# Performance work log

Hardware: AMD Instinct MI355X
Metric: run time of the kernel (lower is better)

Reference implementation:

```python
import jax, jax.numpy as jnp
import numpy as np

H, C = 8, 16            # heads, per-head channels (at_channels)
HID = H * C             # 128
N_NODES = 50000
N_EDGES = 400000
N_GRAPHS = 500
SPEC = 1000


def setup_inputs() -> dict:
    key = jax.random.key(0)
    ks = jax.random.split(key, 32)
    s = 0.05

    def rn(k, shape):
        return jax.random.normal(k, shape, jnp.float32) * s

    inp = {}
    inp["x"] = jax.random.normal(ks[0], (N_NODES, 16), jnp.float32)
    inp["edge_index"] = jax.random.randint(ks[1], (2, N_EDGES), 0, N_NODES, jnp.int32)
    inp["edge_attr"] = jax.random.normal(ks[2], (N_EDGES, 2), jnp.float32)
    inp["batch"] = jnp.sort(jax.random.randint(ks[3], (N_NODES,), 0, N_GRAPHS, jnp.int32))
    # layer 1 (input dim 16)
    inp["at1_Wl"] = rn(ks[4], (16, HID)); inp["at1_bl"] = rn(ks[5], (HID,))
    inp["at1_Wr"] = rn(ks[6], (16, HID)); inp["at1_br"] = rn(ks[7], (HID,))
    inp["at1_We"] = rn(ks[8], (2, HID))
    inp["at1_att"] = rn(ks[9], (H, C))
    inp["at1_bias"] = rn(ks[10], (HID,))
    inp["l1_W"] = rn(ks[11], (16, HID)); inp["l1_b"] = rn(ks[12], (HID,))
    # layers 2..10 stacked (input dim 128)
    inp["atk_Wl"] = rn(ks[13], (9, HID, HID)); inp["atk_bl"] = rn(ks[14], (9, HID))
    inp["atk_Wr"] = rn(ks[15], (9, HID, HID)); inp["atk_br"] = rn(ks[16], (9, HID))
    inp["atk_We"] = rn(ks[17], (9, 2, HID))
    inp["atk_att"] = rn(ks[18], (9, H, C))
    inp["atk_bias"] = rn(ks[19], (9, HID))
    inp["lk_W"] = rn(ks[20], (9, HID, HID)); inp["lk_b"] = rn(ks[21], (9, HID))
    # readout
    inp["lin_W"] = rn(ks[22], (HID, SPEC)); inp["lin_b"] = rn(ks[23], (SPEC,))
    return inp


def _gatv2(x, src, dst, eattr, Wl, bl, Wr, br, We, att, bias):
    """PyG GATv2Conv forward (concat=True, slope=0.2, self-loops already in src/dst)."""
    N = x.shape[0]
    xl = (x @ Wl + bl).reshape(N, H, C)   # source transform
    xr = (x @ Wr + br).reshape(N, H, C)   # target transform
    ee = (eattr @ We).reshape(-1, H, C)   # edge embedding
    m = xl[src] + xr[dst] + ee            # [E, H, C]
    m = jnp.where(m > 0, m, 0.2 * m)      # leaky_relu
    logits = jnp.einsum('ehc,hc->eh', m, att)
    mx = jax.ops.segment_max(logits, dst, num_segments=N)
    ea = jnp.exp(logits - mx[dst])
    denom = jax.ops.segment_sum(ea, dst, num_segments=N)
    alpha = ea / jnp.maximum(denom[dst], 1e-16)
    out = jax.ops.segment_sum(xl[src] * alpha[:, :, None], dst, num_segments=N)
    return out.reshape(N, HID) + bias


def reference(x, edge_index, edge_attr, batch,
              at1_Wl, at1_bl, at1_Wr, at1_br, at1_We, at1_att, at1_bias, l1_W, l1_b,
              atk_Wl, atk_bl, atk_Wr, atk_br, atk_We, atk_att, atk_bias, lk_W, lk_b,
              lin_W, lin_b):
    N = x.shape[0]
    # add self loops once (edge_attr fill_value='mean', PyG default)
    sl = jnp.arange(N, dtype=edge_index.dtype)
    src = jnp.concatenate([edge_index[0], sl])
    dst = jnp.concatenate([edge_index[1], sl])
    ea = jnp.concatenate([edge_attr, jnp.broadcast_to(edge_attr.mean(0), (N, edge_attr.shape[1]))])

    h = jax.nn.elu(_gatv2(x, src, dst, ea, at1_Wl, at1_bl, at1_Wr, at1_br,
                          at1_We, at1_att, at1_bias) + x @ l1_W + l1_b)
    for i in range(9):  # layers 2..10
        h = jax.nn.elu(_gatv2(h, src, dst, ea, atk_Wl[i], atk_bl[i], atk_Wr[i], atk_br[i],
                              atk_We[i], atk_att[i], atk_bias[i]) + h @ lk_W[i] + lk_b[i])

    # global mean pool over graphs
    sums = jax.ops.segment_sum(h, batch, num_segments=N_GRAPHS)
    cnts = jax.ops.segment_sum(jnp.ones((N, 1), h.dtype), batch, num_segments=N_GRAPHS)
    g = sums / jnp.maximum(cnts, 1.0)
    return g @ lin_W + lin_b
```

## Files before the change

### kernel.cpp

```cpp
#include <hip/hip_runtime.h>
#include <hip/hip_bf16.h>
#include <cstdint>

#define HID 128

typedef __attribute__((ext_vector_type(8))) short bf16x8;
typedef __attribute__((ext_vector_type(4))) float f32x4;

__device__ __forceinline__ unsigned short f2bf(float x) {
    __hip_bfloat16 h = __float2bfloat16(x);
    return __builtin_bit_cast(unsigned short, h);
}
__device__ __forceinline__ float bf2f(unsigned short u) {
    return __bfloat162float(__builtin_bit_cast(__hip_bfloat16, u));
}
__device__ __forceinline__ float bflo(unsigned u) {
    return __builtin_bit_cast(float, u << 16);
}
__device__ __forceinline__ float bfhi(unsigned u) {
    return __builtin_bit_cast(float, u & 0xffff0000u);
}
__device__ __forceinline__ float4 ld4bf(const unsigned short* p) {
    ushort4 u = *(const ushort4*)p;
    return make_float4(bf2f(u.x), bf2f(u.y), bf2f(u.z), bf2f(u.w));
}
__device__ __forceinline__ int lower_bound_i(const int* a, int n, int v) {
    int lo = 0, hi = n;
    while (lo < hi) { int m = (lo + hi) >> 1; if (a[m] < v) lo = m + 1; else hi = m; }
    return lo;
}

__global__ __launch_bounds__(256) void mean_kernel(const float* __restrict__ eattr,
                                                   float* __restrict__ meansum, int E) {
    float sx = 0.f, sy = 0.f;
    for (int i = blockIdx.x * 256 + threadIdx.x; i < E; i += gridDim.x * 256) {
        float2 v = *(const float2*)(eattr + 2 * (size_t)i);
        sx += v.x; sy += v.y;
    }
    for (int d = 1; d < 64; d <<= 1) { sx += __shfl_xor(sx, d); sy += __shfl_xor(sy, d); }
    if ((threadIdx.x & 63) == 0) { atomicAdd(&meansum[0], sx); atomicAdd(&meansum[1], sy); }
}

__global__ __launch_bounds__(256) void deg_kernel(const int* __restrict__ ei,
                                                  int* __restrict__ deg, int E, int ET) {
    int e = blockIdx.x * 256 + threadIdx.x;
    if (e >= ET) return;
    int dst = (e < E) ? ei[E + e] : (e - E);
    atomicAdd(&deg[dst], 1);
}

__global__ __launch_bounds__(256) void scanA_kernel(const int* __restrict__ deg,
                                                    int* __restrict__ bsum, int N) {
    __shared__ int ws[4];
    int t = threadIdx.x;
    int base = blockIdx.x * 1024 + t * 4;
    int s = 0;
    #pragma unroll
    for (int j = 0; j < 4; j++) { int idx = base + j; if (idx < N) s += deg[idx]; }
    for (int d = 1; d < 64; d <<= 1) s += __shfl_xor(s, d);
    if ((t & 63) == 0) ws[t >> 6] = s;
    __syncthreads();
    if (t == 0) bsum[blockIdx.x] = ws[0] + ws[1] + ws[2] + ws[3];
}

__global__ __launch_bounds__(64) void scanB_kernel(const int* __restrict__ bsum,
                                                   int* __restrict__ boff,
                                                   int* __restrict__ row_ptr, int NB, int N) {
    int t = threadIdx.x;
    int v = (t < NB) ? bsum[t] : 0;
    int inc = v;
    #pragma unroll
    for (int d = 1; d < 64; d <<= 1) { int u = __shfl_up(inc, d); if (t >= d) inc += u; }
    if (t < NB) boff[t] = inc - v;
    if (t == 63) row_ptr[N] = inc;
}

__global__ __launch_bounds__(256) void scanC_kernel(const int* __restrict__ deg,
                                                    const int* __restrict__ boff,
                                                    int* __restrict__ row_ptr,
                                                    int* __restrict__ cursor, int N) {
    __shared__ int wsum[4];
    int t = threadIdx.x;
    int lane = t & 63, wid = t >> 6;
    int base = blockIdx.x * 1024 + t * 4;
    int v[4]; int s = 0;
    #pragma unroll
    for (int j = 0; j < 4; j++) { int idx = base + j; v[j] = (idx < N) ? deg[idx] : 0; s += v[j]; }
    int inc = s;
    #pragma unroll
    for (int d = 1; d < 64; d <<= 1) { int u = __shfl_up(inc, d); if (lane >= d) inc += u; }
    if (lane == 63) wsum[wid] = inc;
    __syncthreads();
    int woff = 0;
    for (int ww = 0; ww < wid; ww++) woff += wsum[ww];
    int excl = boff[blockIdx.x] + woff + inc - s;
    #pragma unroll
    for (int j = 0; j < 4; j++) {
        int idx = base + j;
        if (idx < N) { row_ptr[idx] = excl; cursor[idx] = excl; }
        excl += v[j];
    }
}

__global__ __launch_bounds__(256) void fill_kernel(const int* __restrict__ ei,
                                                   const float* __restrict__ eattr,
                                                   const float* __restrict__ meansum,
                                                   int* __restrict__ cursor,
                                                   int* __restrict__ csr_src,
                                                   unsigned int* __restrict__ csr_eap,
                                                   int E, int ET) {
    int e = blockIdx.x * 256 + threadIdx.x;
    if (e >= ET) return;
    int src, dst; float2 ea;
    if (e < E) {
        src = ei[e]; dst = ei[E + e];
        ea = *(const float2*)(eattr + 2 * (size_t)e);
    } else {
        src = dst = e - E;
        float inv = 1.0f / (float)E;
        ea.x = meansum[0] * inv; ea.y = meansum[1] * inv;
    }
    unsigned pea = (unsigned)f2bf(ea.x) | ((unsigned)f2bf(ea.y) << 16);
    int pos = atomicAdd(&cursor[dst], 1);
    csr_src[pos] = src;
    csr_eap[pos] = pea;
}

__global__ __launch_bounds__(256) void wprep_kernel(const float* __restrict__ src,
                                                    unsigned short* __restrict__ hi, int total) {
    int idx = blockIdx.x * 256 + threadIdx.x;
    if (idx >= total) return;
    int layer = idx >> 14;
    int rem = idx & 16383;
    int n = rem >> 7, k = rem & 127;
    hi[idx] = f2bf(src[(layer << 14) | (k << 7) | n]);
}

#define LROW 136
__global__ __launch_bounds__(256) void gemm3_kernel(
    const unsigned short* __restrict__ Hb,
    const unsigned short* __restrict__ W0h, const float* __restrict__ b0, unsigned short* __restrict__ o0,
    const unsigned short* __restrict__ W1h, const float* __restrict__ b1, unsigned short* __restrict__ o1,
    const unsigned short* __restrict__ W2h, const float* __restrict__ b2, unsigned short* __restrict__ o2,
    int N) {
    __shared__ unsigned short lds_h[128 * LROW];
    int tid = threadIdx.x;
    int wid = tid >> 6, lane = tid & 63;
    int row0 = blockIdx.x * 64 + wid * 16;
    int lr = lane & 15;
    int cgrp = lane >> 4;
    int kb = cgrp * 8;
    bool rowsok = (row0 < N);

    bf16x8 ha[4];
    {
        int node = row0 + lr;
        int nodec = rowsok ? ((node < N) ? node : (N - 1)) : 0;
        const unsigned short* pa = Hb + (size_t)nodec * HID + kb;
        #pragma unroll
        for (int kf = 0; kf < 4; kf++) ha[kf] = *(const bf16x8*)(pa + kf * 32);
    }

    const unsigned short* Whs[3] = {W0h, W1h, W2h};
    const float* Bs[3] = {b0, b1, b2};
    unsigned short* Os[3] = {o0, o1, o2};

    for (int w = 0; w < 3; w++) {
        if (w) __syncthreads();
        const unsigned short* sh = Whs[w];
        #pragma unroll
        for (int j = 0; j < 8; j++) {
            int c = tid + 256 * j;
            int r = c >> 4, col = (c & 15) * 8;
            *(bf16x8*)&lds_h[r * LROW + col] = *(const bf16x8*)(sh + r * HID + col);
        }
        __syncthreads();
        if (!rowsok) continue;

        const float* bias = Bs[w];
        unsigned short* outp = Os[w];
        #pragma unroll 2
        for (int nf = 0; nf < 8; nf++) {
            int wrow = nf * 16 + lr;
            const unsigned short* ph = &lds_h[wrow * LROW + kb];
            bf16x8 wf[4];
            #pragma unroll
            for (int kf = 0; kf < 4; kf++) wf[kf] = *(const bf16x8*)(ph + kf * 32);
            f32x4 acc = {0.f, 0.f, 0.f, 0.f};
            #pragma unroll
            for (int kf = 0; kf < 4; kf++)
                acc = __builtin_amdgcn_mfma_f32_16x16x32_bf16(wf[kf], ha[kf], acc, 0, 0, 0);
            int chb = nf * 16 + cgrp * 4;
            float4 bias4 = *(const float4*)(bias + chb);
            int node = row0 + lr;
            ushort4 u;
            u.x = f2bf(acc[0] + bias4.x); u.y = f2bf(acc[1] + bias4.y);
            u.z = f2bf(acc[2] + bias4.z); u.w = f2bf(acc[3] + bias4.w);
            if (node < N) *(ushort4*)(outp + (size_t)node * HID + chb) = u;
        }
    }
}

__global__ __launch_bounds__(256) void transform16_kernel(
    const float* __restrict__ Hin,
    const float* __restrict__ W0, const float* __restrict__ b0, float* __restrict__ o0,
    const float* __restrict__ W1, const float* __restrict__ b1, float* __restrict__ o1,
    int N) {
    constexpr int K = 16;
    __shared__ float Ws[K][HID];
    __shared__ float Hs[32][K + 4];

    const float* W; const float* bias; float* outp;
    if (blockIdx.z == 0) { W = W0; bias = b0; outp = o0; }
    else                 { W = W1; bias = b1; outp = o1; }

    int row0 = blockIdx.x * 32;
    int tid = threadIdx.x;
    int tx = tid & 15, ty = tid >> 4;

    for (int i = tid; i < 32 * (K / 4); i += 256) {
        int r = i / (K / 4), kq = i % (K / 4);
        int row = row0 + r;
        float4 v = make_float4(0.f, 0.f, 0.f, 0.f);
        if (row < N) v = *(const float4*)(Hin + (size_t)row * K + kq * 4);
        *(float4*)&Hs[r][kq * 4] = v;
    }
    for (int i = tid; i < K * 32; i += 256) {
        int k = i >> 5, cq = i & 31;
        *(float4*)&Ws[k][cq * 4] = *(const float4*)(W + (size_t)k * HID + cq * 4);
    }
    __syncthreads();

    float acc[2][8];
    #pragma unroll
    for (int i = 0; i < 2; i++)
        #pragma unroll
        for (int j = 0; j < 8; j++) acc[i][j] = 0.f;

    int r0 = ty * 2, r1 = ty * 2 + 1;
    #pragma unroll
    for (int k = 0; k < K; k++) {
        float a0 = Hs[r0][k];
        float a1 = Hs[r1][k];
        float4 w0 = *(float4*)&Ws[k][tx * 4];
        float4 w1 = *(float4*)&Ws[k][64 + tx * 4];
        acc[0][0] += a0 * w0.x; acc[0][1] += a0 * w0.y; acc[0][2] += a0 * w0.z; acc[0][3] += a0 * w0.w;
        acc[0][4] += a0 * w1.x; acc[0][5] += a0 * w1.y; acc[0][6] += a0 * w1.z; acc[0][7] += a0 * w1.w;
        acc[1][0] += a1 * w0.x; acc[1][1] += a1 * w0.y; acc[1][2] += a1 * w0.z; acc[1][3] += a1 * w0.w;
        acc[1][4] += a1 * w1.x; acc[1][5] += a1 * w1.y; acc[1][6] += a1 * w1.z; acc[1][7] += a1 * w1.w;
    }

    float4 bb0 = *(const float4*)(bias + tx * 4);
    float4 bb1 = *(const float4*)(bias + 64 + tx * 4);
    #pragma unroll
    for (int i = 0; i < 2; i++) {
        int row = row0 + ty * 2 + i;
        if (row < N) {
            float4 v0 = make_float4(acc[i][0] + bb0.x, acc[i][1] + bb0.y, acc[i][2] + bb0.z, acc[i][3] + bb0.w);
            float4 v1 = make_float4(acc[i][4] + bb1.x, acc[i][5] + bb1.y, acc[i][6] + bb1.z, acc[i][7] + bb1.w);
            *(float4*)(outp + (size_t)row * HID + tx * 4) = v0;
            *(float4*)(outp + (size_t)row * HID + 64 + tx * 4) = v1;
        }
    }
}

__global__ __launch_bounds__(256) void combine16_kernel(
    const float* __restrict__ Hin,
    const float* __restrict__ W, const float* __restrict__ bias,
    const float* __restrict__ Att, unsigned short* __restrict__ Hb,
    int N) {
    constexpr int K = 16;
    __shared__ float Ws[K][HID];
    __shared__ float Hs[32][K + 4];

    int row0 = blockIdx.x * 32;
    int tid = threadIdx.x;
    int tx = tid & 15, ty = tid >> 4;

    for (int i = tid; i < 32 * (K / 4); i += 256) {
        int r = i / (K / 4), kq = i % (K / 4);
        int row = row0 + r;
        float4 v = make_float4(0.f, 0.f, 0.f, 0.f);
        if (row < N) v = *(const float4*)(Hin + (size_t)row * K + kq * 4);
        *(float4*)&Hs[r][kq * 4] = v;
    }
    for (int i = tid; i < K * 32; i += 256) {
        int k = i >> 5, cq = i & 31;
        *(float4*)&Ws[k][cq * 4] = *(const float4*)(W + (size_t)k * HID + cq * 4);
    }
    __syncthreads();

    float acc[2][8];
    #pragma unroll
    for (int i = 0; i < 2; i++)
        #pragma unroll
        for (int j = 0; j < 8; j++) acc[i][j] = 0.f;

    int r0 = ty * 2, r1 = ty * 2 + 1;
    #pragma unroll
    for (int k = 0; k < K; k++) {
        float a0 = Hs[r0][k];
        float a1 = Hs[r1][k];
        float4 w0 = *(float4*)&Ws[k][tx * 4];
        float4 w1 = *(float4*)&Ws[k][64 + tx * 4];
        acc[0][0] += a0 * w0.x; acc[0][1] += a0 * w0.y; acc[0][2] += a0 * w0.z; acc[0][3] += a0 * w0.w;
        acc[0][4] += a0 * w1.x; acc[0][5] += a0 * w1.y; acc[0][6] += a0 * w1.z; acc[0][7] += a0 * w1.w;
        acc[1][0] += a1 * w0.x; acc[1][1] += a1 * w0.y; acc[1][2] += a1 * w0.z; acc[1][3] += a1 * w0.w;
        acc[1][4] += a1 * w1.x; acc[1][5] += a1 * w1.y; acc[1][6] += a1 * w1.z; acc[1][7] += a1 * w1.w;
    }

    float4 bb0 = *(const float4*)(bias + tx * 4);
    float4 bb1 = *(const float4*)(bias + 64 + tx * 4);
    #pragma unroll
    for (int i = 0; i < 2; i++) {
        int row = row0 + ty * 2 + i;
        if (row < N) {
            const float* p0 = Att + (size_t)row * HID + tx * 4;
            float4 g0 = *(const float4*)p0;
            float4 g1 = *(const float4*)(p0 + 64);
            float v[8];
            v[0] = g0.x + acc[i][0] + bb0.x; v[1] = g0.y + acc[i][1] + bb0.y;
            v[2] = g0.z + acc[i][2] + bb0.z; v[3] = g0.w + acc[i][3] + bb0.w;
            v[4] = g1.x + acc[i][4] + bb1.x; v[5] = g1.y + acc[i][5] + bb1.y;
            v[6] = g1.z + acc[i][6] + bb1.z; v[7] = g1.w + acc[i][7] + bb1.w;
            #pragma unroll
            for (int j = 0; j < 8; j++) v[j] = (v[j] > 0.f) ? v[j] : (__expf(v[j]) - 1.f);
            ushort4 h0, h1;
            h0.x = f2bf(v[0]); h0.y = f2bf(v[1]); h0.z = f2bf(v[2]); h0.w = f2bf(v[3]);
            h1.x = f2bf(v[4]); h1.y = f2bf(v[5]); h1.z = f2bf(v[6]); h1.w = f2bf(v[7]);
            *(ushort4*)(Hb + (size_t)row * HID + tx * 4) = h0;
            *(ushort4*)(Hb + (size_t)row * HID + 64 + tx * 4) = h1;
        }
    }
}

template <int FUSE>
__global__ __launch_bounds__(256) void edge_kernel(
    const void* __restrict__ XLv, const void* __restrict__ XRv,
    const int* __restrict__ row_ptr, const int* __restrict__ csr_src,
    const unsigned int* __restrict__ csr_eap,
    const float* __restrict__ att,
    const float* __restrict__ We,
    const float* __restrict__ gbias,
    const unsigned short* __restrict__ lin,
    float* __restrict__ hf, unsigned short* __restrict__ hb,
    int N) {
    int n = (blockIdx.x * 256 + threadIdx.x) >> 6;
    int lane = threadIdx.x & 63;
    int half = lane >> 5;
    int l = lane & 31;
    bool active = (n < N);
    int nn = active ? n : 0;

    int c0 = l * 4;
    float4 av  = *(const float4*)(att + c0);
    float4 we0 = *(const float4*)(We + c0);
    float4 we1 = *(const float4*)(We + HID + c0);

    auto ldx = [&](const void* p, int idx) -> float4 {
        if constexpr (FUSE) return ld4bf((const unsigned short*)p + (size_t)idx * HID + c0);
        else                return *(const float4*)((const float*)p + (size_t)idx * HID + c0);
    };
    float4 xr = ldx(XRv, nn);

    int eb = 0, eend = 0;
    if (active) { eb = row_ptr[n]; eend = row_ptr[n + 1]; }
    int mid = (eb + eend + 1) >> 1;
    int sb = half ? mid : eb;
    int se = half ? eend : mid;

    float l_run = 0.f;
    float4 fa = make_float4(0.f, 0.f, 0.f, 0.f);

    for (int base = sb; base < se; base += 32) {
        int cnt = min(32, se - base);
        int myi = base + l;
        int msrc = 0; unsigned mea = 0;
        if (myi < se) { msrc = csr_src[myi]; mea = csr_eap[myi]; }

        int s0 = __shfl(msrc, 0, 32);
        int s1 = __shfl(msrc, 1, 32);
        unsigned e0 = __shfl(mea, 0, 32);
        unsigned e1 = __shfl(mea, 1, 32);
        float4 xl0 = ldx(XLv, s0);
        float4 xl1 = ldx(XLv, s1);

        for (int j = 0; ; j += 2) {
            bool more = (j + 2 < cnt);
            int ns0 = 0, ns1 = 0; unsigned ne0 = 0, ne1 = 0;
            float4 nxl0, nxl1;
            if (more) {
                ns0 = __shfl(msrc, j + 2, 32);
                ns1 = __shfl(msrc, j + 3, 32);
                ne0 = __shfl(mea, j + 2, 32);
                ne1 = __shfl(mea, j + 3, 32);
                nxl0 = ldx(XLv, ns0);
                nxl1 = ldx(XLv, ns1);
            }
            float ex0 = bflo(e0), ey0 = bfhi(e0);
            float ex1 = bflo(e1), ey1 = bfhi(e1);
            float t, part0, part1;
            float m0x = xl0.x + xr.x + ex0 * we0.x + ey0 * we1.x;
            float m0y = xl0.y + xr.y + ex0 * we0.y + ey0 * we1.y;
            float m0z = xl0.z + xr.z + ex0 * we0.z + ey0 * we1.z;
            float m0w = xl0.w + xr.w + ex0 * we0.w + ey0 * we1.w;
            m0x = fmaxf(m0x, 0.2f * m0x);
            m0y = fmaxf(m0y, 0.2f * m0y);
            m0z = fmaxf(m0z, 0.2f * m0z);
            m0w = fmaxf(m0w, 0.2f * m0w);
            part0 = m0x * av.x + m0y * av.y + m0z * av.z + m0w * av.w;
            float m1x = xl1.x + xr.x + ex1 * we0.x + ey1 * we1.x;
            float m1y = xl1.y + xr.y + ex1 * we0.y + ey1 * we1.y;
            float m1z = xl1.z + xr.z + ex1 * we0.z + ey1 * we1.z;
            float m1w = xl1.w + xr.w + ex1 * we0.w + ey1 * we1.w;
            m1x = fmaxf(m1x, 0.2f * m1x);
            m1y = fmaxf(m1y, 0.2f * m1y);
            m1z = fmaxf(m1z, 0.2f * m1z);
            m1w = fmaxf(m1w, 0.2f * m1w);
            part1 = m1x * av.x + m1y * av.y + m1z * av.z + m1w * av.w;
            t = __shfl_xor(part0, 1); part0 += t;
            t = __shfl_xor(part0, 2); part0 += t;
            t = __shfl_xor(part1, 1); part1 += t;
            t = __shfl_xor(part1, 2); part1 += t;

            bool two = (j + 1 < cnt);
            float p0 = __expf(fminf(part0, 60.f));
            float p1 = two ? __expf(fminf(part1, 60.f)) : 0.f;
            l_run += p0 + p1;
            fa.x += p0 * xl0.x + p1 * xl1.x;
            fa.y += p0 * xl0.y + p1 * xl1.y;
            fa.z += p0 * xl0.z + p1 * xl1.z;
            fa.w += p0 * xl0.w + p1 * xl1.w;
            if (!more) break;
            s0 = ns0; s1 = ns1; e0 = ne0; e1 = ne1; xl0 = nxl0; xl1 = nxl1;
        }
    }

    l_run += __shfl_xor(l_run, 32);
    fa.x += __shfl_xor(fa.x, 32);
    fa.y += __shfl_xor(fa.y, 32);
    fa.z += __shfl_xor(fa.z, 32);
    fa.w += __shfl_xor(fa.w, 32);

    if (!active || half) return;
    float inv = 1.f / fmaxf(l_run, 1e-16f);
    float4 bias4 = *(const float4*)(gbias + c0);
    float4 v;
    v.x = fa.x * inv + bias4.x;
    v.y = fa.y * inv + bias4.y;
    v.z = fa.z * inv + bias4.z;
    v.w = fa.w * inv + bias4.w;
    if constexpr (FUSE) {
        float4 lv = ld4bf(lin + (size_t)n * HID + c0);
        v.x += lv.x; v.y += lv.y; v.z += lv.z; v.w += lv.w;
        v.x = (v.x > 0.f) ? v.x : (__expf(v.x) - 1.f);
        v.y = (v.y > 0.f) ? v.y : (__expf(v.y) - 1.f);
        v.z = (v.z > 0.f) ? v.z : (__expf(v.z) - 1.f);
        v.w = (v.w > 0.f) ? v.w : (__expf(v.w) - 1.f);
        if (hf) *(float4*)(hf + (size_t)n * HID + c0) = v;
        ushort4 hh;
        hh.x = f2bf(v.x); hh.y = f2bf(v.y); hh.z = f2bf(v.z); hh.w = f2bf(v.w);
        *(ushort4*)(hb + (size_t)n * HID + c0) = hh;
    } else {
        *(float4*)(hf + (size_t)n * HID + c0) = v;
    }
}

__global__ __launch_bounds__(128) void pool_kernel(const float* __restrict__ h,
                                                   const int* __restrict__ batch,
                                                   float* __restrict__ g, int N) {
    int gid = blockIdx.x;
    int lo = lower_bound_i(batch, N, gid);
    int hi = lower_bound_i(batch, N, gid + 1);
    int c = threadIdx.x;
    float s = 0.f;
    for (int i = lo; i < hi; i++) s += h[(size_t)i * HID + c];
    g[gid * HID + c] = s / fmaxf((float)(hi - lo), 1.0f);
}

__global__ __launch_bounds__(256) void readout_kernel(const float* __restrict__ g,
                                                      const float* __restrict__ W,
                                                      const float* __restrict__ b,
                                                      float* __restrict__ out, int S) {
    __shared__ float gs[HID];
    int gid = blockIdx.y;
    if (threadIdx.x < HID) gs[threadIdx.x] = g[gid * HID + threadIdx.x];
    __syncthreads();
    int c = blockIdx.x * 256 + threadIdx.x;
    if (c < S) {
        float acc = b[c];
        #pragma unroll 8
        for (int k = 0; k < HID; k++) acc += gs[k] * W[(size_t)k * S + c];
        out[(size_t)gid * S + c] = acc;
    }
}

extern "C" void kernel_launch(void* const* d_in, const int* in_sizes, int n_in,
                              void* d_out, int out_size, void* d_ws, size_t ws_size,
                              hipStream_t stream) {
    const float* x      = (const float*)d_in[0];
    const int*   ei     = (const int*)d_in[1];
    const float* eattr  = (const float*)d_in[2];
    const int*   batch  = (const int*)d_in[3];
    const float* at1_Wl = (const float*)d_in[4];
    const float* at1_bl = (const float*)d_in[5];
    const float* at1_Wr = (const float*)d_in[6];
    const float* at1_br = (const float*)d_in[7];
    const float* at1_We = (const float*)d_in[8];
    const float* at1_att= (const float*)d_in[9];
    const float* at1_b  = (const float*)d_in[10];
    const float* l1_W   = (const float*)d_in[11];
    const float* l1_b   = (const float*)d_in[12];
    const float* atk_Wl = (const float*)d_in[13];
    const float* atk_bl = (const float*)d_in[14];
    const float* atk_Wr = (const float*)d_in[15];
    const float* atk_br = (const float*)d_in[16];
    const float* atk_We = (const float*)d_in[17];
    const float* atk_att= (const float*)d_in[18];
    const float* atk_b  = (const float*)d_in[19];
    const float* lk_W   = (const float*)d_in[20];
    const float* lk_b   = (const float*)d_in[21];
    const float* lin_W  = (const float*)d_in[22];
    const float* lin_b  = (const float*)d_in[23];
    float* out = (float*)d_out;

    const int N  = in_sizes[0] / 16;
    const int E  = in_sizes[1] / 2;
    const int ET = E + N;
    const int S  = 1000;
    const int G  = out_size / S;

    char* w = (char*)d_ws;
    auto alloc = [&](size_t bytes) -> char* {
        char* p = w; w += (bytes + 255) & ~(size_t)255; return p;
    };
    float*  XLf     = (float*)alloc((size_t)N * HID * 4);
    float*  XRf     = (float*)alloc((size_t)N * HID * 4);
    unsigned short* XLb = (unsigned short*)alloc((size_t)N * HID * 2);
    unsigned short* XRb = (unsigned short*)alloc((size_t)N * HID * 2);
    unsigned short* Linb = (unsigned short*)alloc((size_t)N * HID * 2);
    float*  Hf      = (float*)alloc((size_t)N * HID * 4);
    unsigned short* Hb = (unsigned short*)alloc((size_t)N * HID * 2);
    int*    deg     = (int*)alloc((size_t)N * 4);
    int*    row_ptr = (int*)alloc((size_t)(N + 1) * 4);
    int*    cursor  = (int*)alloc((size_t)N * 4);
    int*    csr_src = (int*)alloc((size_t)ET * 4);
    unsigned int* csr_eap = (unsigned int*)alloc((size_t)ET * 4);
    float*  meansum = (float*)alloc(8);
    int*    bsum    = (int*)alloc(256);
    int*    boff    = (int*)alloc(256);
    unsigned short* WlTh = (unsigned short*)alloc((size_t)9 * 16384 * 2);
    unsigned short* WrTh = (unsigned short*)alloc((size_t)9 * 16384 * 2);
    unsigned short* WkTh = (unsigned short*)alloc((size_t)9 * 16384 * 2);
    float*  gpool   = (float*)alloc((size_t)G * HID * 4);
    (void)ws_size; (void)n_in;

    hipMemsetAsync(deg, 0, (size_t)N * 4, stream);
    hipMemsetAsync(meansum, 0, 8, stream);

    const int wtot = 9 * 16384;
    wprep_kernel<<<(wtot + 255) / 256, 256, 0, stream>>>(atk_Wl, WlTh, wtot);
    wprep_kernel<<<(wtot + 255) / 256, 256, 0, stream>>>(atk_Wr, WrTh, wtot);
    wprep_kernel<<<(wtot + 255) / 256, 256, 0, stream>>>(lk_W,   WkTh, wtot);

    mean_kernel<<<256, 256, 0, stream>>>(eattr, meansum, E);
    deg_kernel<<<(ET + 255) / 256, 256, 0, stream>>>(ei, deg, E, ET);
    const int NB = (N + 1023) / 1024;
    scanA_kernel<<<NB, 256, 0, stream>>>(deg, bsum, N);
    scanB_kernel<<<1, 64, 0, stream>>>(bsum, boff, row_ptr, NB, N);
    scanC_kernel<<<NB, 256, 0, stream>>>(deg, boff, row_ptr, cursor, N);
    fill_kernel<<<(ET + 255) / 256, 256, 0, stream>>>(ei, eattr, meansum, cursor, csr_src, csr_eap, E, ET);

    const int gx16 = (N + 31) / 32;
    const int ge   = (N + 3) / 4;
    const int gx3  = (N + 63) / 64;

    transform16_kernel<<<dim3(gx16, 1, 2), 256, 0, stream>>>(x, at1_Wl, at1_bl, XLf, at1_Wr, at1_br, XRf, N);
    edge_kernel<0><<<ge, 256, 0, stream>>>(XLf, XRf, row_ptr, csr_src, csr_eap, at1_att, at1_We, at1_b,
                                           nullptr, Hf, nullptr, N);
    combine16_kernel<<<gx16, 256, 0, stream>>>(x, l1_W, l1_b, Hf, Hb, N);

    for (int i = 0; i < 9; i++) {
        const unsigned short* wlh = WlTh + (size_t)i * 16384;
        const unsigned short* wrh = WrTh + (size_t)i * 16384;
        const unsigned short* wkh = WkTh + (size_t)i * 16384;
        const float* bl = atk_bl + (size_t)i * HID;
        const float* br = atk_br + (size_t)i * HID;
        const float* bk = lk_b   + (size_t)i * HID;
        const float* Wep = atk_We + (size_t)i * 2 * HID;
        const float* at = atk_att + (size_t)i * HID;
        const float* ab = atk_b  + (size_t)i * HID;

        gemm3_kernel<<<gx3, 256, 0, stream>>>(Hb,
                                              wlh, bl, XLb,
                                              wrh, br, XRb,
                                              wkh, bk, Linb, N);
        edge_kernel<1><<<ge, 256, 0, stream>>>(XLb, XRb, row_ptr, csr_src, csr_eap, at, Wep, ab,
                                               Linb, (i == 8) ? Hf : nullptr, Hb, N);
    }

    pool_kernel<<<G, 128, 0, stream>>>(Hf, batch, gpool, N);
    readout_kernel<<<dim3((S + 255) / 256, G), 256, 0, stream>>>(gpool, lin_W, lin_b, out, S);
}
```

Measured before the change: 754.9 us.

## Switch intermediate storage from bf16 to fp16 and use packed-half math in edge kernel

Changes all 16-bit intermediates (weights, node features, edge attributes) from bf16 to fp16 and the GEMM MFMA to the f16 variant. The edge kernel for layers 2-10 is split into its own version that computes the message, leaky-relu and attention dot product with packed half2 arithmetic and fdot2. This is meant to halve the VALU work of the per-edge logit computation. It reduces dynamic range, so large activations could overflow, and it lowers precision in the attention logits.

```diff
diff --git a/kernel.cpp b/kernel.cpp
--- a/kernel.cpp
+++ b/kernel.cpp
@@ -1,28 +1,30 @@
 #include <hip/hip_runtime.h>
-#include <hip/hip_bf16.h>
+#include <hip/hip_fp16.h>
 #include <cstdint>
 
 #define HID 128
 
-typedef __attribute__((ext_vector_type(8))) short bf16x8;
+typedef __attribute__((ext_vector_type(8))) _Float16 f16x8;
+typedef __attribute__((ext_vector_type(2))) _Float16 h2v;
 typedef __attribute__((ext_vector_type(4))) float f32x4;
 
-__device__ __forceinline__ unsigned short f2bf(float x) {
-    __hip_bfloat16 h = __float2bfloat16(x);
-    return __builtin_bit_cast(unsigned short, h);
-}
-__device__ __forceinline__ float bf2f(unsigned short u) {
-    return __bfloat162float(__builtin_bit_cast(__hip_bfloat16, u));
-}
-__device__ __forceinline__ float bflo(unsigned u) {
-    return __builtin_bit_cast(float, u << 16);
-}
-__device__ __forceinline__ float bfhi(unsigned u) {
-    return __builtin_bit_cast(float, u & 0xffff0000u);
-}
-__device__ __forceinline__ float4 ld4bf(const unsigned short* p) {
-    ushort4 u = *(const ushort4*)p;
-    return make_float4(bf2f(u.x), bf2f(u.y), bf2f(u.z), bf2f(u.w));
+__device__ __forceinline__ unsigned short f2h(float x) {
+    return __builtin_bit_cast(unsigned short, (_Float16)x);
+}
+__device__ __forceinline__ float h2f(unsigned short u) {
+    return (float)__builtin_bit_cast(_Float16, u);
+}
+__device__ __forceinline__ h2v mkh2(unsigned short a, unsigned short b) {
+    unsigned v = (unsigned)a | ((unsigned)b << 16);
+    return __builtin_bit_cast(h2v, v);
+}
+__device__ __forceinline__ h2v splath(unsigned short a) {
+    _Float16 h = __builtin_bit_cast(_Float16, a);
+    h2v r; r[0] = h; r[1] = h;
+    return r;
+}
+__device__ __forceinline__ float fdot2v(h2v a, h2v b, float c) {
+    return __builtin_amdgcn_fdot2(a, b, c, false);
 }
 __device__ __forceinline__ int lower_bound_i(const int* a, int n, int v) {
     int lo = 0, hi = n;
@@ -120,7 +122,7 @@
         float inv = 1.0f / (float)E;
         ea.x = meansum[0] * inv; ea.y = meansum[1] * inv;
     }
-    unsigned pea = (unsigned)f2bf(ea.x) | ((unsigned)f2bf(ea.y) << 16);
+    unsigned pea = (unsigned)f2h(ea.x) | ((unsigned)f2h(ea.y) << 16);
     int pos = atomicAdd(&cursor[dst], 1);
     csr_src[pos] = src;
     csr_eap[pos] = pea;
@@ -133,7 +135,7 @@
     int layer = idx >> 14;
     int rem = idx & 16383;
     int n = rem >> 7, k = rem & 127;
-    hi[idx] = f2bf(src[(layer << 14) | (k << 7) | n]);
+    hi[idx] = f2h(src[(layer << 14) | (k << 7) | n]);
 }
 
 #define LROW 136
@@ -152,13 +154,13 @@
     int kb = cgrp * 8;
     bool rowsok = (row0 < N);
 
-    bf16x8 ha[4];
+    f16x8 ha[4];
     {
         int node = row0 + lr;
         int nodec = rowsok ? ((node < N) ? node : (N - 1)) : 0;
         const unsigned short* pa = Hb + (size_t)nodec * HID + kb;
         #pragma unroll
-        for (int kf = 0; kf < 4; kf++) ha[kf] = *(const bf16x8*)(pa + kf * 32);
+        for (int kf = 0; kf < 4; kf++) ha[kf] = *(const f16x8*)(pa + kf * 32);
     }
 
     const unsigned short* Whs[3] = {W0h, W1h, W2h};
@@ -172,7 +174,7 @@
         for (int j = 0; j < 8; j++) {
             int c = tid + 256 * j;
             int r = c >> 4, col = (c & 15) * 8;
-            *(bf16x8*)&lds_h[r * LROW + col] = *(const bf16x8*)(sh + r * HID + col);
+            *(f16x8*)&lds_h[r * LROW + col] = *(const f16x8*)(sh + r * HID + col);
         }
         __syncthreads();
         if (!rowsok) continue;
@@ -183,19 +185,19 @@
         for (int nf = 0; nf < 8; nf++) {
             int wrow = nf * 16 + lr;
             const unsigned short* ph = &lds_h[wrow * LROW + kb];
-            bf16x8 wf[4];
+            f16x8 wf[4];
             #pragma unroll
-            for (int kf = 0; kf < 4; kf++) wf[kf] = *(const bf16x8*)(ph + kf * 32);
+            for (int kf = 0; kf < 4; kf++) wf[kf] = *(const f16x8*)(ph + kf * 32);
             f32x4 acc = {0.f, 0.f, 0.f, 0.f};
             #pragma unroll
             for (int kf = 0; kf < 4; kf++)
-                acc = __builtin_amdgcn_mfma_f32_16x16x32_bf16(wf[kf], ha[kf], acc, 0, 0, 0);
+                acc = __builtin_amdgcn_mfma_f32_16x16x32_f16(wf[kf], ha[kf], acc, 0, 0, 0);
             int chb = nf * 16 + cgrp * 4;
             float4 bias4 = *(const float4*)(bias + chb);
             int node = row0 + lr;
             ushort4 u;
-            u.x = f2bf(acc[0] + bias4.x); u.y = f2bf(acc[1] + bias4.y);
-            u.z = f2bf(acc[2] + bias4.z); u.w = f2bf(acc[3] + bias4.w);
+            u.x = f2h(acc[0] + bias4.x); u.y = f2h(acc[1] + bias4.y);
+            u.z = f2h(acc[2] + bias4.z); u.w = f2h(acc[3] + bias4.w);
             if (node < N) *(ushort4*)(outp + (size_t)node * HID + chb) = u;
         }
     }
@@ -326,25 +328,22 @@
             #pragma unroll
             for (int j = 0; j < 8; j++) v[j] = (v[j] > 0.f) ? v[j] : (__expf(v[j]) - 1.f);
             ushort4 h0, h1;
-            h0.x = f2bf(v[0]); h0.y = f2bf(v[1]); h0.z = f2bf(v[2]); h0.w = f2bf(v[3]);
-            h1.x = f2bf(v[4]); h1.y = f2bf(v[5]); h1.z = f2bf(v[6]); h1.w = f2bf(v[7]);
+            h0.x = f2h(v[0]); h0.y = f2h(v[1]); h0.z = f2h(v[2]); h0.w = f2h(v[3]);
+            h1.x = f2h(v[4]); h1.y = f2h(v[5]); h1.z = f2h(v[6]); h1.w = f2h(v[7]);
             *(ushort4*)(Hb + (size_t)row * HID + tx * 4) = h0;
             *(ushort4*)(Hb + (size_t)row * HID + 64 + tx * 4) = h1;
         }
     }
 }
 
-template <int FUSE>
-__global__ __launch_bounds__(256) void edge_kernel(
-    const void* __restrict__ XLv, const void* __restrict__ XRv,
+__global__ __launch_bounds__(256) void edge1_kernel(
+    const float* __restrict__ XL, const float* __restrict__ XR,
     const int* __restrict__ row_ptr, const int* __restrict__ csr_src,
     const unsigned int* __restrict__ csr_eap,
     const float* __restrict__ att,
     const float* __restrict__ We,
     const float* __restrict__ gbias,
-    const unsigned short* __restrict__ lin,
-    float* __restrict__ hf, unsigned short* __restrict__ hb,
-    int N) {
+    float* __restrict__ hf, int N) {
     int n = (blockIdx.x * 256 + threadIdx.x) >> 6;
     int lane = threadIdx.x & 63;
     int half = lane >> 5;
@@ -356,12 +355,7 @@
     float4 av  = *(const float4*)(att + c0);
     float4 we0 = *(const float4*)(We + c0);
     float4 we1 = *(const float4*)(We + HID + c0);
-
-    auto ldx = [&](const void* p, int idx) -> float4 {
-        if constexpr (FUSE) return ld4bf((const unsigned short*)p + (size_t)idx * HID + c0);
-        else                return *(const float4*)((const float*)p + (size_t)idx * HID + c0);
-    };
-    float4 xr = ldx(XRv, nn);
+    float4 xr  = *(const float4*)(XR + (size_t)nn * HID + c0);
 
     int eb = 0, eend = 0;
     if (active) { eb = row_ptr[n]; eend = row_ptr[n + 1]; }
@@ -382,8 +376,8 @@
         int s1 = __shfl(msrc, 1, 32);
         unsigned e0 = __shfl(mea, 0, 32);
         unsigned e1 = __shfl(mea, 1, 32);
-        float4 xl0 = ldx(XLv, s0);
-        float4 xl1 = ldx(XLv, s1);
+        float4 xl0 = *(const float4*)(XL + (size_t)s0 * HID + c0);
+        float4 xl1 = *(const float4*)(XL + (size_t)s1 * HID + c0);
 
         for (int j = 0; ; j += 2) {
             bool more = (j + 2 < cnt);
@@ -394,11 +388,11 @@
                 ns1 = __shfl(msrc, j + 3, 32);
                 ne0 = __shfl(mea, j + 2, 32);
                 ne1 = __shfl(mea, j + 3, 32);
-                nxl0 = ldx(XLv, ns0);
-                nxl1 = ldx(XLv, ns1);
+                nxl0 = *(const float4*)(XL + (size_t)ns0 * HID + c0);
+                nxl1 = *(const float4*)(XL + (size_t)ns1 * HID + c0);
             }
-            float ex0 = bflo(e0), ey0 = bfhi(e0);
-            float ex1 = bflo(e1), ey1 = bfhi(e1);
+            float ex0 = h2f(e0 & 0xffff), ey0 = h2f(e0 >> 16);
+            float ex1 = h2f(e1 & 0xffff), ey1 = h2f(e1 >> 16);
             float t, part0, part1;
             float m0x = xl0.x + xr.x + ex0 * we0.x + ey0 * we1.x;
             float m0y = xl0.y + xr.y + ex0 * we0.y + ey0 * we1.y;
@@ -450,20 +444,136 @@
     v.y = fa.y * inv + bias4.y;
     v.z = fa.z * inv + bias4.z;
     v.w = fa.w * inv + bias4.w;
-    if constexpr (FUSE) {
-        float4 lv = ld4bf(lin + (size_t)n * HID + c0);
-        v.x += lv.x; v.y += lv.y; v.z += lv.z; v.w += lv.w;
-        v.x = (v.x > 0.f) ? v.x : (__expf(v.x) - 1.f);
-        v.y = (v.y > 0.f) ? v.y : (__expf(v.y) - 1.f);
-        v.z = (v.z > 0.f) ? v.z : (__expf(v.z) - 1.f);
-        v.w = (v.w > 0.f) ? v.w : (__expf(v.w) - 1.f);
-        if (hf) *(float4*)(hf + (size_t)n * HID + c0) = v;
-        ushort4 hh;
-        hh.x = f2bf(v.x); hh.y = f2bf(v.y); hh.z = f2bf(v.z); hh.w = f2bf(v.w);
-        *(ushort4*)(hb + (size_t)n * HID + c0) = hh;
-    } else {
-        *(float4*)(hf + (size_t)n * HID + c0) = v;
-    }
+    *(float4*)(hf + (size_t)n * HID + c0) = v;
+}
+
+__global__ __launch_bounds__(256) void edgeh_kernel(
+    const unsigned short* __restrict__ XL, const unsigned short* __restrict__ XR,
+    const int* __restrict__ row_ptr, const int* __restrict__ csr_src,
+    const unsigned int* __restrict__ csr_eap,
+    const float* __restrict__ att,
+    const float* __restrict__ We,
+    const float* __restrict__ gbias,
+    const unsigned short* __restrict__ lin,
+    float* __restrict__ hf, unsigned short* __restrict__ hb,
+    int N) {
+    int n = (blockIdx.x * 256 + threadIdx.x) >> 6;
+    int lane = threadIdx.x & 63;
+    int half = lane >> 5;
+    int l = lane & 31;
+    bool active = (n < N);
+    int nn = active ? n : 0;
+
+    int c0 = l * 4;
+    float4 avf = *(const float4*)(att + c0);
+    float4 w0f = *(const float4*)(We + c0);
+    float4 w1f = *(const float4*)(We + HID + c0);
+    h2v avA; avA[0] = (_Float16)avf.x; avA[1] = (_Float16)avf.y;
+    h2v avB; avB[0] = (_Float16)avf.z; avB[1] = (_Float16)avf.w;
+    h2v weA0; weA0[0] = (_Float16)w0f.x; weA0[1] = (_Float16)w0f.y;
+    h2v weB0; weB0[0] = (_Float16)w0f.z; weB0[1] = (_Float16)w0f.w;
+    h2v weA1; weA1[0] = (_Float16)w1f.x; weA1[1] = (_Float16)w1f.y;
+    h2v weB1; weB1[0] = (_Float16)w1f.z; weB1[1] = (_Float16)w1f.w;
+    h2v k02; k02[0] = (_Float16)0.2f; k02[1] = (_Float16)0.2f;
+
+    ushort4 xru = *(const ushort4*)(XR + (size_t)nn * HID + c0);
+    h2v xrA = mkh2(xru.x, xru.y), xrB = mkh2(xru.z, xru.w);
+
+    int eb = 0, eend = 0;
+    if (active) { eb = row_ptr[n]; eend = row_ptr[n + 1]; }
+    int mid = (eb + eend + 1) >> 1;
+    int sb = half ? mid : eb;
+    int se = half ? eend : mid;
+
+    float l_run = 0.f;
+    float4 fa = make_float4(0.f, 0.f, 0.f, 0.f);
+
+    for (int base = sb; base < se; base += 32) {
+        int cnt = min(32, se - base);
+        int myi = base + l;
+        int msrc = 0; unsigned mea = 0;
+        if (myi < se) { msrc = csr_src[myi]; mea = csr_eap[myi]; }
+
+        int s0 = __shfl(msrc, 0, 32);
+        int s1 = __shfl(msrc, 1, 32);
+        unsigned e0 = __shfl(mea, 0, 32);
+        unsigned e1 = __shfl(mea, 1, 32);
+        ushort4 u0 = *(const ushort4*)(XL + (size_t)s0 * HID + c0);
+        ushort4 u1 = *(const ushort4*)(XL + (size_t)s1 * HID + c0);
+
+        for (int j = 0; ; j += 2) {
+            bool more = (j + 2 < cnt);
+            int ns0 = 0, ns1 = 0; unsigned ne0 = 0, ne1 = 0;
+            ushort4 nu0, nu1;
+            if (more) {
+                ns0 = __shfl(msrc, j + 2, 32);
+                ns1 = __shfl(msrc, j + 3, 32);
+                ne0 = __shfl(mea, j + 2, 32);
+                ne1 = __shfl(mea, j + 3, 32);
+                nu0 = *(const ushort4*)(XL + (size_t)ns0 * HID + c0);
+                nu1 = *(const ushort4*)(XL + (size_t)ns1 * HID + c0);
+            }
+            h2v ex0 = splath((unsigned short)(e0 & 0xffff));
+            h2v ey0 = splath((unsigned short)(e0 >> 16));
+            h2v ex1 = splath((unsigned short)(e1 & 0xffff));
+            h2v ey1 = splath((unsigned short)(e1 >> 16));
+            h2v xl0A = mkh2(u0.x, u0.y), xl0B = mkh2(u0.z, u0.w);
+            h2v xl1A = mkh2(u1.x, u1.y), xl1B = mkh2(u1.z, u1.w);
+
+            h2v mA = xl0A + xrA + ex0 * weA0 + ey0 * weA1;
+            mA = __builtin_elementwise_max(mA, k02 * mA);
+            h2v mB = xl0B + xrB + ex0 * weB0 + ey0 * weB1;
+            mB = __builtin_elementwise_max(mB, k02 * mB);
+            float part0 = fdot2v(mB, avB, fdot2v(mA, avA, 0.f));
+
+            h2v nA = xl1A + xrA + ex1 * weA0 + ey1 * weA1;
+            nA = __builtin_elementwise_max(nA, k02 * nA);
+            h2v nB = xl1B + xrB + ex1 * weB0 + ey1 * weB1;
+            nB = __builtin_elementwise_max(nB, k02 * nB);
+            float part1 = fdot2v(nB, avB, fdot2v(nA, avA, 0.f));
+
+            float t;
+            t = __shfl_xor(part0, 1); part0 += t;
+            t = __shfl_xor(part0, 2); part0 += t;
+            t = __shfl_xor(part1, 1); part1 += t;
+            t = __shfl_xor(part1, 2); part1 += t;
+
+            bool two = (j + 1 < cnt);
+            float p0 = __expf(fminf(part0, 60.f));
+            float p1 = two ? __expf(fminf(part1, 60.f)) : 0.f;
+            l_run += p0 + p1;
+            fa.x += p0 * h2f(u0.x) + p1 * h2f(u1.x);
+            fa.y += p0 * h2f(u0.y) + p1 * h2f(u1.y);
+            fa.z += p0 * h2f(u0.z) + p1 * h2f(u1.z);
+            fa.w += p0 * h2f(u0.w) + p1 * h2f(u1.w);
+            if (!more) break;
+            s0 = ns0; s1 = ns1; e0 = ne0; e1 = ne1; u0 = nu0; u1 = nu1;
+        }
+    }
+
+    l_run += __shfl_xor(l_run, 32);
+    fa.x += __shfl_xor(fa.x, 32);
+    fa.y += __shfl_xor(fa.y, 32);
+    fa.z += __shfl_xor(fa.z, 32);
+    fa.w += __shfl_xor(fa.w, 32);
+
+    if (!active || half) return;
+    float inv = 1.f / fmaxf(l_run, 1e-16f);
+    float4 bias4 = *(const float4*)(gbias + c0);
+    ushort4 lu = *(const ushort4*)(lin + (size_t)n * HID + c0);
+    float4 v;
+    v.x = fa.x * inv + bias4.x + h2f(lu.x);
+    v.y = fa.y * inv + bias4.y + h2f(lu.y);
+    v.z = fa.z * inv + bias4.z + h2f(lu.z);
+    v.w = fa.w * inv + bias4.w + h2f(lu.w);
+    v.x = (v.x > 0.f) ? v.x : (__expf(v.x) - 1.f);
+    v.y = (v.y > 0.f) ? v.y : (__expf(v.y) - 1.f);
+    v.z = (v.z > 0.f) ? v.z : (__expf(v.z) - 1.f);
+    v.w = (v.w > 0.f) ? v.w : (__expf(v.w) - 1.f);
+    if (hf) *(float4*)(hf + (size_t)n * HID + c0) = v;
+    ushort4 hh;
+    hh.x = f2h(v.x); hh.y = f2h(v.y); hh.z = f2h(v.z); hh.w = f2h(v.w);
+    *(ushort4*)(hb + (size_t)n * HID + c0) = hh;
 }
 
 __global__ __launch_bounds__(128) void pool_kernel(const float* __restrict__ h,
@@ -555,8 +665,9 @@
     float*  gpool   = (float*)alloc((size_t)G * HID * 4);
     (void)ws_size; (void)n_in;
 
-    hipMemsetAsync(deg, 0, (size_t)N * 4, stream);
-    hipMemsetAsync(meansum, 0, 8, stream);
+    hipError_t err;
+    err = hipMemsetAsync(deg, 0, (size_t)N * 4, stream); (void)err;
+    err = hipMemsetAsync(meansum, 0, 8, stream); (void)err;
 
     const int wtot = 9 * 16384;
     wprep_kernel<<<(wtot + 255) / 256, 256, 0, stream>>>(atk_Wl, WlTh, wtot);
@@ -576,8 +687,7 @@
     const int gx3  = (N + 63) / 64;
 
     transform16_kernel<<<dim3(gx16, 1, 2), 256, 0, stream>>>(x, at1_Wl, at1_bl, XLf, at1_Wr, at1_br, XRf, N);
-    edge_kernel<0><<<ge, 256, 0, stream>>>(XLf, XRf, row_ptr, csr_src, csr_eap, at1_att, at1_We, at1_b,
-                                           nullptr, Hf, nullptr, N);
+    edge1_kernel<<<ge, 256, 0, stream>>>(XLf, XRf, row_ptr, csr_src, csr_eap, at1_att, at1_We, at1_b, Hf, N);
     combine16_kernel<<<gx16, 256, 0, stream>>>(x, l1_W, l1_b, Hf, Hb, N);
 
     for (int i = 0; i < 9; i++) {
@@ -595,8 +705,8 @@
                                               wlh, bl, XLb,
                                               wrh, br, XRb,
                                               wkh, bk, Linb, N);
-        edge_kernel<1><<<ge, 256, 0, stream>>>(XLb, XRb, row_ptr, csr_src, csr_eap, at, Wep, ab,
-                                               Linb, (i == 8) ? Hf : nullptr, Hb, N);
+        edgeh_kernel<<<ge, 256, 0, stream>>>(XLb, XRb, row_ptr, csr_src, csr_eap, at, Wep, ab,
+                                             Linb, (i == 8) ? Hf : nullptr, Hb, N);
     }
 
     pool_kernel<<<G, 128, 0, stream>>>(Hf, batch, gpool, N);
```

Result: faster. 708.5 us (-6.2%).
